# Optimization experiments

Measured on AMD Instinct MI355X. Metric: run time of the kernel, lower is better.

The kernel has to match this reference:

```python
import jax, jax.numpy as jnp
import numpy as np
import math

B, C, HH, WW = 4, 256, 64, 64
NUM_HEADS = 4
GROUPS = 8
EPS = 1e-5


def setup_inputs() -> dict:
    key = jax.random.key(0)
    k1, k2, k3 = jax.random.split(key, 3)
    x = jax.random.normal(k1, (B, C, HH, WW), dtype=jnp.float32)
    gn_w = jnp.ones((C,), dtype=jnp.float32)
    gn_b = jnp.zeros((C,), dtype=jnp.float32)
    qkv_w = jax.random.normal(k2, (3 * C, C), dtype=jnp.float32) * (1.0 / math.sqrt(C))
    qkv_b = jnp.zeros((3 * C,), dtype=jnp.float32)
    proj_w = jax.random.normal(k3, (C, C), dtype=jnp.float32) * (1.0 / math.sqrt(C))
    proj_b = jnp.zeros((C,), dtype=jnp.float32)
    return {"x": x, "gn_w": gn_w, "gn_b": gn_b, "qkv_w": qkv_w,
            "qkv_b": qkv_b, "proj_w": proj_w, "proj_b": proj_b}


def reference(x, gn_w, gn_b, qkv_w, qkv_b, proj_w, proj_b):
    b, c, h, w = x.shape
    nh = NUM_HEADS
    d = c // nh          # head dim = 64
    s = h * w            # sequence length = 4096

    # GroupNorm(8, c): normalize over (c//G, h, w) per group, biased variance
    xg = x.reshape(b, GROUPS, c // GROUPS, h, w)
    mu = xg.mean(axis=(2, 3, 4), keepdims=True)
    var = xg.var(axis=(2, 3, 4), keepdims=True)
    xn = ((xg - mu) * jax.lax.rsqrt(var + EPS)).reshape(b, c, h, w)
    xn = xn * gn_w[None, :, None, None] + gn_b[None, :, None, None]

    # 1x1 conv QKV == channel-wise matmul
    qkv = jnp.einsum('oc,bchw->bohw', qkv_w, xn) + qkv_b[None, :, None, None]
    qkv = qkv.reshape(b, 3, nh, d, s)
    q = jnp.transpose(qkv[:, 0], (0, 1, 3, 2))  # [b, nh, s, d]
    k = jnp.transpose(qkv[:, 1], (0, 1, 3, 2))
    v = jnp.transpose(qkv[:, 2], (0, 1, 3, 2))

    scale = 1.0 / math.sqrt(d)
    attn = jnp.einsum('bhqd,bhkd->bhqk', q, k) * scale  # [b, nh, s, s]
    attn = jax.nn.softmax(attn, axis=-1)
    out = jnp.einsum('bhqk,bhkd->bhqd', attn, v)        # [b, nh, s, d]

    out = jnp.transpose(out, (0, 1, 3, 2)).reshape(b, c, h, w)
    out = jnp.einsum('oc,bchw->bohw', proj_w, out) + proj_b[None, :, None, None]
    return out + x
```

## Files before the change

kernel.cpp:

```cpp
#include <hip/hip_runtime.h>
#include <hip/hip_bf16.h>

#define B_ 4
#define C_ 256
#define S_ 4096
#define NH_ 4
#define HD_ 64
#define LOG2E 1.4426950408889634f
#define QSC 0.18033688011112042f

typedef __attribute__((ext_vector_type(8))) short short8;
typedef __attribute__((ext_vector_type(4))) short short4v;
typedef __attribute__((ext_vector_type(4))) float f32x4;
typedef __attribute__((ext_vector_type(16))) float f32x16;
typedef __attribute__((ext_vector_type(4))) unsigned uint4v;

static __device__ __forceinline__ short f2bf(float f) {
  unsigned u = __builtin_bit_cast(unsigned, f);
  u += 0x7fffu + ((u >> 16) & 1u);
  return (short)(u >> 16);
}
static __device__ __forceinline__ float bf2f(short h) {
  unsigned u = ((unsigned)(unsigned short)h) << 16;
  return __builtin_bit_cast(float, u);
}

#if __has_builtin(__builtin_amdgcn_exp2f)
#define EXP2(x) __builtin_amdgcn_exp2f(x)
#else
#define EXP2(x) exp2f(x)
#endif

static __device__ __forceinline__ unsigned pkbf(float a, float b) {
  unsigned r;
  asm("v_cvt_pk_bf16_f32 %0, %1, %2" : "=v"(r) : "v"(a), "v"(b));
  return r;
}
static __device__ __forceinline__ void pl32swap(unsigned& a, unsigned& b) {
  asm volatile("v_permlane32_swap_b32 %0, %1" : "+v"(a), "+v"(b));
}
static __device__ __forceinline__ void gl_lds16(const short* g, char* l) {
  __builtin_amdgcn_global_load_lds(
      (const __attribute__((address_space(1))) void*)g,
      (__attribute__((address_space(3))) void*)l, 16, 0, 0);
}

__global__ __launch_bounds__(256) void k_pre(const float* __restrict__ x,
                                             const float* __restrict__ wq,
                                             const float* __restrict__ wp,
                                             float* __restrict__ part,
                                             short* __restrict__ oq,
                                             short* __restrict__ op) {
  int t = threadIdx.x;
  const float* p = x + (size_t)blockIdx.x * 16384;
  float s = 0.f, ss = 0.f;
  const float4* p4 = reinterpret_cast<const float4*>(p);
  for (int i = t; i < 4096; i += 256) {
    float4 v = p4[i];
    s += v.x + v.y + v.z + v.w;
    ss += v.x * v.x + v.y * v.y + v.z * v.z + v.w * v.w;
  }
  for (int m = 1; m < 64; m <<= 1) {
    s += __shfl_xor(s, m, 64);
    ss += __shfl_xor(ss, m, 64);
  }
  __shared__ float rs[4], rss[4];
  int w = t >> 6;
  if ((t & 63) == 0) { rs[w] = s; rss[w] = ss; }
  {
    int i = (blockIdx.x * 256 + t) * 4;
    const int n1 = 768 * 256;
    float sc = 1.f;
    const float* src;
    short* dst;
    if (i < n1) {
      src = wq + i; dst = oq + i;
      if (i < 256 * 256) sc = QSC;
    } else {
      src = wp + (i - n1); dst = op + (i - n1);
    }
    float4 v = *reinterpret_cast<const float4*>(src);
    short4v o;
    o[0] = f2bf(v.x * sc); o[1] = f2bf(v.y * sc);
    o[2] = f2bf(v.z * sc); o[3] = f2bf(v.w * sc);
    *reinterpret_cast<short4v*>(dst) = o;
  }
  __syncthreads();
  if (t == 0) {
    part[2 * blockIdx.x] = rs[0] + rs[1] + rs[2] + rs[3];
    part[2 * blockIdx.x + 1] = rss[0] + rss[1] + rss[2] + rss[3];
  }
}

__global__ __launch_bounds__(256) void k_gn_apply(const float* __restrict__ x,
                                                  const float* __restrict__ gw,
                                                  const float* __restrict__ gb,
                                                  const float* __restrict__ part,
                                                  short* __restrict__ xnt) {
  int st = blockIdx.x;
  int ct = blockIdx.y;
  int b = blockIdx.z;
  int t = threadIdx.x;
  __shared__ short T[64 * 72];
  __shared__ float smu[2], sri[2];
  int c0 = ct * 64, s0 = st * 64;
  if (t < 2) {
    int g = (c0 >> 5) + t;
    int base = b * 64 + g * 8;
    float s = 0.f, ss = 0.f;
    for (int j = 0; j < 8; j++) {
      s += part[2 * (base + j)];
      ss += part[2 * (base + j) + 1];
    }
    float inv = 1.f / (32.f * S_);
    float mu = s * inv;
    float var = ss * inv - mu * mu;
    smu[t] = mu;
    sri[t] = rsqrtf(var + 1e-5f);
  }
  __syncthreads();
  int r4 = t >> 4;
  int f4 = t & 15;
  for (int p = 0; p < 4; p++) {
    int r = p * 16 + r4;
    int c = c0 + r;
    int gl = r >> 5;
    float mu = smu[gl];
    float ri = sri[gl];
    float A = gw[c] * ri;
    float Bb = gb[c] - mu * A;
    float4 v = *reinterpret_cast<const float4*>(x + ((size_t)(b * C_ + c)) * S_ + s0 + f4 * 4);
    int sb = f4 * 4;
    T[(sb + 0) * 72 + r] = f2bf(v.x * A + Bb);
    T[(sb + 1) * 72 + r] = f2bf(v.y * A + Bb);
    T[(sb + 2) * 72 + r] = f2bf(v.z * A + Bb);
    T[(sb + 3) * 72 + r] = f2bf(v.w * A + Bb);
  }
  __syncthreads();
  for (int it = 0; it < 2; it++) {
    int cch = t + it * 256;
    int sl = cch >> 3, c8 = cch & 7;
    short8 v = *reinterpret_cast<short8*>(&T[sl * 72 + c8 * 8]);
    *reinterpret_cast<short8*>(xnt + ((size_t)(b * S_ + s0 + sl)) * C_ + c0 + c8 * 8) = v;
  }
}

template <int MODE, int NSP>
__global__ __launch_bounds__(256) void k_gemm(const short* __restrict__ Wbf,
                                              const short* __restrict__ Xt,
                                              const float* __restrict__ bias,
                                              const float* __restrict__ xres,
                                              short* __restrict__ q_sd,
                                              short* __restrict__ k_sd,
                                              short* __restrict__ v_ds,
                                              long op_stride,
                                              const float* __restrict__ lbufg,
                                              float* __restrict__ outp) {
  int tn = blockIdx.x;
  int tm = blockIdx.y;
  int b = blockIdx.z;
  int t = threadIdx.x;
  __shared__ short lds[4 * 64 * 72];
  char* glds = (char*)lds;
  short* Blp = lds + 4096;
  int w = t >> 6, lane = t & 63;
  int wr = w >> 1, wc = w & 1;
  int l15 = lane & 15, l4 = lane >> 4;
  int wbg = __builtin_amdgcn_readfirstlane(w) << 10;

  f32x4 acc[4][4];
  for (int m = 0; m < 4; m++)
    for (int n = 0; n < 4; n++)
      for (int j = 0; j < 4; j++) acc[m][n][j] = 0.f;

  const short* Arow = Wbf + (size_t)(tm * 128) * 256;
  const short* Brow = Xt + ((size_t)b * S_ + tn * 128) * 256;

  int r0 = t >> 2, c40 = t & 3;
  int sw0 = (c40 ^ ((r0 >> 1) & 3)) * 8;
  int r1 = (t + 256) >> 2;
  int sw1 = (c40 ^ ((r1 >> 1) & 3)) * 8;

  if (MODE == 0) {
    gl_lds16(Arow + (size_t)r0 * 256 + sw0, glds + wbg);
    gl_lds16(Arow + (size_t)r1 * 256 + sw1, glds + 4096 + wbg);
    gl_lds16(Brow + (size_t)r0 * 256 + sw0, glds + 8192 + wbg);
    gl_lds16(Brow + (size_t)r1 * 256 + sw1, glds + 12288 + wbg);
    asm volatile("s_waitcnt vmcnt(0)" ::: "memory");
    __builtin_amdgcn_s_barrier();
    asm volatile("" ::: "memory");
    for (int step = 0; step < 8; step++) {
      char* cb = glds + ((step & 1) << 14);
      if (step + 1 < 8) {
        char* nb = glds + (((step + 1) & 1) << 14);
        int kk = (step + 1) * 32;
        gl_lds16(Arow + (size_t)r0 * 256 + kk + sw0, nb + wbg);
        gl_lds16(Arow + (size_t)r1 * 256 + kk + sw1, nb + 4096 + wbg);
        gl_lds16(Brow + (size_t)r0 * 256 + kk + sw0, nb + 8192 + wbg);
        gl_lds16(Brow + (size_t)r1 * 256 + kk + sw1, nb + 12288 + wbg);
      }
      short8 af[4], bf[4];
      for (int mt = 0; mt < 4; mt++) {
        int row = wr * 64 + mt * 16 + l15;
        af[mt] = *reinterpret_cast<short8*>(cb + row * 64 + ((l4 ^ ((row >> 1) & 3)) << 4));
      }
      for (int nt = 0; nt < 4; nt++) {
        int row = wc * 64 + nt * 16 + l15;
        bf[nt] = *reinterpret_cast<short8*>(cb + 8192 + row * 64 + ((l4 ^ ((row >> 1) & 3)) << 4));
      }
      for (int mt = 0; mt < 4; mt++)
        for (int nt = 0; nt < 4; nt++)
          acc[mt][nt] =
              __builtin_amdgcn_mfma_f32_16x16x32_bf16(af[mt], bf[nt], acc[mt][nt], 0, 0, 0);
      if (step + 1 < 8) {
        asm volatile("s_waitcnt vmcnt(0)" ::: "memory");
        __builtin_amdgcn_s_barrier();
        asm volatile("" ::: "memory");
      }
    }
  } else {
    for (int kk = 0; kk < 256; kk += 32) {
      __syncthreads();
      gl_lds16(Arow + (size_t)r0 * 256 + kk + sw0, glds + wbg);
      gl_lds16(Arow + (size_t)r1 * 256 + kk + sw1, glds + 4096 + wbg);
      for (int i = 0; i < 2; i++) {
        int cch = t + i * 256;
        int r = cch >> 2, c4 = cch & 3;
        int c = kk + c4 * 8;
        int bh2 = b * 4 + (c >> 6);
        int d = c & 63;
        int s_glob = tn * 128 + r;
        size_t ro = ((size_t)bh2 * S_ + s_glob) * HD_ + d;
        float a8[8] = {0.f, 0.f, 0.f, 0.f, 0.f, 0.f, 0.f, 0.f};
        float l = 0.f;
#pragma unroll
        for (int i2 = 0; i2 < NSP; i2++) {
          short8 pv = *reinterpret_cast<const short8*>(Xt + (size_t)i2 * op_stride + ro);
#pragma unroll
          for (int j = 0; j < 8; j++) a8[j] += bf2f(pv[j]);
          l += lbufg[(size_t)(i2 * 16 + bh2) * S_ + s_glob];
        }
        float inv = 1.f / l;
        short8 vbv;
#pragma unroll
        for (int j = 0; j < 8; j++) vbv[j] = f2bf(a8[j] * inv);
        *reinterpret_cast<short8*>(&Blp[r * 40 + c4 * 8]) = vbv;
      }
      asm volatile("s_waitcnt vmcnt(0)" ::: "memory");
      __syncthreads();

      short8 af[4], bf[4];
      for (int mt = 0; mt < 4; mt++) {
        int row = wr * 64 + mt * 16 + l15;
        af[mt] = *reinterpret_cast<short8*>(glds + row * 64 + ((l4 ^ ((row >> 1) & 3)) << 4));
      }
      for (int nt = 0; nt < 4; nt++) {
        int row = wc * 64 + nt * 16 + l15;
        bf[nt] = *reinterpret_cast<short8*>(&Blp[row * 40 + l4 * 8]);
      }
      for (int mt = 0; mt < 4; mt++)
        for (int nt = 0; nt < 4; nt++)
          acc[mt][nt] =
              __builtin_amdgcn_mfma_f32_16x16x32_bf16(af[mt], bf[nt], acc[mt][nt], 0, 0, 0);
    }
  }
  __syncthreads();

  if (MODE == 0) {
    int o_base = tm * 128 + wr * 64;
    int tt = o_base >> 8;
    int h = (o_base >> 6) & 3;
    int s_base = tn * 128 + wc * 64;
    int bh = b * NH_ + h;
    if (tt == 2) {
      for (int mt = 0; mt < 4; mt++)
        for (int nt = 0; nt < 4; nt++)
          for (int i = 0; i < 4; i++) {
            int o = o_base + mt * 16 + l4 * 4 + i;
            int dd = o & 63;
            int s = s_base + nt * 16 + l15;
            float val = acc[mt][nt][i] + bias[o];
            v_ds[((size_t)bh * HD_ + dd) * S_ + s] = f2bf(val);
          }
    } else {
      float bsc = (tt == 0) ? QSC : 1.f;
      short* T = lds + w * (64 * 72);
      for (int mt = 0; mt < 4; mt++)
        for (int nt = 0; nt < 4; nt++)
          for (int i = 0; i < 4; i++) {
            int o = o_base + mt * 16 + l4 * 4 + i;
            int dd = mt * 16 + l4 * 4 + i;
            int sl = nt * 16 + l15;
            float val = acc[mt][nt][i] + bias[o] * bsc;
            T[sl * 72 + dd] = f2bf(val);
          }
      short* dst = (tt == 0) ? q_sd : k_sd;
      for (int it = 0; it < 8; it++) {
        int cch = lane + it * 64;
        int sl = cch >> 3, c8 = cch & 7;
        short8 v = *reinterpret_cast<short8*>(&T[sl * 72 + c8 * 8]);
        *reinterpret_cast<short8*>(dst + ((size_t)bh * S_ + s_base + sl) * HD_ + c8 * 8) = v;
      }
    }
  } else {
    for (int mt = 0; mt < 4; mt++) {
      int o = tm * 128 + wr * 64 + mt * 16 + l4 * 4;
      for (int nt = 0; nt < 4; nt++) {
        int s = tn * 128 + wc * 64 + nt * 16 + l15;
        for (int i = 0; i < 4; i++) {
          size_t off = ((size_t)(b * C_ + o + i)) * S_ + s;
          outp[off] = acc[mt][nt][i] + bias[o + i] + xres[off];
        }
      }
    }
  }
}

__global__ __launch_bounds__(256, 2) void k_attn(const short* __restrict__ q_sd,
                                                 const short* __restrict__ k_sd,
                                                 const short* __restrict__ v_ds,
                                                 short* __restrict__ op_base,
                                                 long op_stride,
                                                 float* __restrict__ lbuf,
                                                 int ntile) {
  int bid = blockIdx.x;
  int qt = bid >> 5;
  int bh = (bid >> 1) & 15;
  int sk = bid & 1;
  int t = threadIdx.x, w = t >> 6, lane = t & 63;
  int l31 = lane & 31, hi = lane >> 5, hi8 = hi * 8;
  int qb = qt * 256 + w * 64;

  __shared__ char smem[49152];

  int wb = __builtin_amdgcn_readfirstlane(w) << 10;

  int r8 = t >> 3, s8 = t & 7;
  int sw8 = (s8 ^ (r8 & 7)) * 8;
  const short* kb = k_sd + ((size_t)bh * S_ + (size_t)sk * ntile * 64) * HD_;
  const short* vbg = v_ds + (size_t)bh * HD_ * S_ + sk * ntile * 64;
  int koff0 = r8 * 64 + sw8;
  int koff1 = koff0 + 32 * 64;
  size_t voff0 = (size_t)r8 * S_ + sw8;
  size_t voff1 = voff0 + (size_t)32 * S_;

#define STAGE(bsel, ti)                                                        \
  do {                                                                         \
    const short* kt_ = kb + (size_t)(ti) * (64 * HD_);                         \
    const short* vt_ = vbg + (ti) * 64;                                        \
    char* lb_ = smem + ((bsel) << 14) + wb;                                    \
    gl_lds16(kt_ + koff0, lb_);                                                \
    gl_lds16(kt_ + koff1, lb_ + 4096);                                         \
    gl_lds16(vt_ + voff0, lb_ + 8192);                                         \
    gl_lds16(vt_ + voff1, lb_ + 12288);                                        \
  } while (0)

  const short* qpA = q_sd + ((size_t)bh * S_ + qb + l31) * HD_ + hi8;
  short8 qfA[4], qfB[4];
#pragma unroll
  for (int sl = 0; sl < 4; sl++) {
    qfA[sl] = *reinterpret_cast<const short8*>(qpA + sl * 16);
    qfB[sl] = *reinterpret_cast<const short8*>(qpA + 32 * HD_ + sl * 16);
  }

  int x7 = l31 & 7;
  int rb0 = l31 * 128;

  f32x16 OA0, OA1, OB0, OB1;
#pragma unroll
  for (int r = 0; r < 16; r++) { OA0[r] = 0.f; OA1[r] = 0.f; OB0[r] = 0.f; OB1[r] = 0.f; }
  float lA = 0.f, lB = 0.f;

  STAGE(0, 0);
  if (ntile > 1) STAGE(1, 1);
  asm volatile("s_waitcnt vmcnt(4)" ::: "memory");
  __builtin_amdgcn_s_barrier();
  asm volatile("" ::: "memory");

#define MKPA(pa, s0, s1)                                                       \
  do {                                                                         \
    unsigned c0 = pkbf(s0[0], s0[1]), c1 = pkbf(s0[2], s0[3]);                 \
    unsigned c2 = pkbf(s0[4], s0[5]), c3 = pkbf(s0[6], s0[7]);                 \
    pl32swap(c0, c2); pl32swap(c1, c3);                                        \
    uint4v u0; u0[0] = c0; u0[1] = c1; u0[2] = c2; u0[3] = c3;                 \
    pa[0] = __builtin_bit_cast(short8, u0);                                    \
    unsigned c4 = pkbf(s0[8], s0[9]), c5 = pkbf(s0[10], s0[11]);               \
    unsigned c6 = pkbf(s0[12], s0[13]), c7 = pkbf(s0[14], s0[15]);             \
    pl32swap(c4, c6); pl32swap(c5, c7);                                        \
    uint4v u1; u1[0] = c4; u1[1] = c5; u1[2] = c6; u1[3] = c7;                 \
    pa[1] = __builtin_bit_cast(short8, u1);                                    \
    unsigned d0 = pkbf(s1[0], s1[1]), d1 = pkbf(s1[2], s1[3]);                 \
    unsigned d2 = pkbf(s1[4], s1[5]), d3 = pkbf(s1[6], s1[7]);                 \
    pl32swap(d0, d2); pl32swap(d1, d3);                                        \
    uint4v u2; u2[0] = d0; u2[1] = d1; u2[2] = d2; u2[3] = d3;                 \
    pa[2] = __builtin_bit_cast(short8, u2);                                    \
    unsigned d4 = pkbf(s1[8], s1[9]), d5 = pkbf(s1[10], s1[11]);               \
    unsigned d6 = pkbf(s1[12], s1[13]), d7 = pkbf(s1[14], s1[15]);             \
    pl32swap(d4, d6); pl32swap(d5, d7);                                        \
    uint4v u3; u3[0] = d4; u3[1] = d5; u3[2] = d6; u3[3] = d7;                 \
    pa[3] = __builtin_bit_cast(short8, u3);                                    \
  } while (0)

  int cs = 0;
  for (int it = 0; it < ntile; it++) {
    char* cur = smem + (cs << 14);
    int ns = (cs == 2) ? 0 : cs + 1;
    int ps = (cs == 0) ? 2 : cs - 1;
    if (it + 2 < ntile) STAGE(ps, it + 2);

    f32x16 sA0, sA1, sB0, sB1;
#pragma unroll
    for (int r = 0; r < 16; r++) { sA0[r] = 0.f; sA1[r] = 0.f; sB0[r] = 0.f; sB1[r] = 0.f; }
    __builtin_amdgcn_s_setprio(1);
#pragma unroll
    for (int sl = 0; sl < 4; sl++) {
      int so = ((sl * 2 + hi) ^ x7) << 4;
      short8 kf0 = *reinterpret_cast<short8*>(cur + rb0 + so);
      short8 kf1 = *reinterpret_cast<short8*>(cur + 4096 + rb0 + so);
      sA0 = __builtin_amdgcn_mfma_f32_32x32x16_bf16(kf0, qfA[sl], sA0, 0, 0, 0);
      sB0 = __builtin_amdgcn_mfma_f32_32x32x16_bf16(kf0, qfB[sl], sB0, 0, 0, 0);
      sA1 = __builtin_amdgcn_mfma_f32_32x32x16_bf16(kf1, qfA[sl], sA1, 0, 0, 0);
      sB1 = __builtin_amdgcn_mfma_f32_32x32x16_bf16(kf1, qfB[sl], sB1, 0, 0, 0);
    }
    __builtin_amdgcn_s_setprio(0);

#pragma unroll
    for (int r = 0; r < 16; r++) sA0[r] = EXP2(sA0[r]);
#pragma unroll
    for (int r = 0; r < 16; r++) sA1[r] = EXP2(sA1[r]);
#pragma unroll
    for (int r = 0; r < 16; r++) sB0[r] = EXP2(sB0[r]);
#pragma unroll
    for (int r = 0; r < 16; r++) sB1[r] = EXP2(sB1[r]);
    {
      float a0 = 0.f, a1 = 0.f, a2 = 0.f, a3 = 0.f;
      float b0 = 0.f, b1 = 0.f, b2 = 0.f, b3 = 0.f;
#pragma unroll
      for (int r = 0; r < 16; r += 4) {
        a0 += sA0[r]; a1 += sA0[r + 1]; a2 += sA0[r + 2]; a3 += sA0[r + 3];
        a0 += sA1[r]; a1 += sA1[r + 1]; a2 += sA1[r + 2]; a3 += sA1[r + 3];
        b0 += sB0[r]; b1 += sB0[r + 1]; b2 += sB0[r + 2]; b3 += sB0[r + 3];
        b0 += sB1[r]; b1 += sB1[r + 1]; b2 += sB1[r + 2]; b3 += sB1[r + 3];
      }
      float rsA = (a0 + a1) + (a2 + a3);
      float rsB = (b0 + b1) + (b2 + b3);
      rsA += __shfl_xor(rsA, 32, 64);
      rsB += __shfl_xor(rsB, 32, 64);
      lA += rsA;
      lB += rsB;
    }

    short8 paA[4], paB[4];
    MKPA(paA, sA0, sA1);
    MKPA(paB, sB0, sB1);

    __builtin_amdgcn_s_setprio(1);
#pragma unroll
    for (int ks = 0; ks < 4; ks++) {
      int so = ((ks * 2 + hi) ^ x7) << 4;
      short8 vf0 = *reinterpret_cast<short8*>(cur + 8192 + rb0 + so);
      short8 vf1 = *reinterpret_cast<short8*>(cur + 12288 + rb0 + so);
      OA0 = __builtin_amdgcn_mfma_f32_32x32x16_bf16(vf0, paA[ks], OA0, 0, 0, 0);
      OB0 = __builtin_amdgcn_mfma_f32_32x32x16_bf16(vf0, paB[ks], OB0, 0, 0, 0);
      OA1 = __builtin_amdgcn_mfma_f32_32x32x16_bf16(vf1, paA[ks], OA1, 0, 0, 0);
      OB1 = __builtin_amdgcn_mfma_f32_32x32x16_bf16(vf1, paB[ks], OB1, 0, 0, 0);
    }
    __builtin_amdgcn_s_setprio(0);

    if (it + 1 < ntile) {
      if (it + 2 < ntile)
        asm volatile("s_waitcnt vmcnt(4)" ::: "memory");
      else
        asm volatile("s_waitcnt vmcnt(0)" ::: "memory");
      __builtin_amdgcn_s_barrier();
      asm volatile("" ::: "memory");
    }
    cs = ns;
  }

  short* optrA = op_base + (size_t)sk * op_stride + ((size_t)bh * S_ + qb + l31) * HD_;
  short* optrB = optrA + 32 * HD_;
#pragma unroll
  for (int qd = 0; qd < 4; qd++) {
    short4v a0, a1, b0v, b1v;
#pragma unroll
    for (int i = 0; i < 4; i++) {
      a0[i] = f2bf(OA0[qd * 4 + i]);
      a1[i] = f2bf(OA1[qd * 4 + i]);
      b0v[i] = f2bf(OB0[qd * 4 + i]);
      b1v[i] = f2bf(OB1[qd * 4 + i]);
    }
    int d0 = qd * 8 + hi * 4;
    *reinterpret_cast<short4v*>(optrA + d0) = a0;
    *reinterpret_cast<short4v*>(optrA + 32 + d0) = a1;
    *reinterpret_cast<short4v*>(optrB + d0) = b0v;
    *reinterpret_cast<short4v*>(optrB + 32 + d0) = b1v;
  }
  if (hi == 0) {
    lbuf[(size_t)(sk * 16 + bh) * S_ + qb + l31] = lA;
    lbuf[(size_t)(sk * 16 + bh) * S_ + qb + 32 + l31] = lB;
  }
#undef STAGE
#undef MKPA
}

extern "C" void kernel_launch(void* const* d_in, const int* in_sizes, int n_in,
                              void* d_out, int out_size, void* d_ws, size_t ws_size,
                              hipStream_t stream) {
  const float* x      = (const float*)d_in[0];
  const float* gn_w   = (const float*)d_in[1];
  const float* gn_b   = (const float*)d_in[2];
  const float* qkv_w  = (const float*)d_in[3];
  const float* qkv_b  = (const float*)d_in[4];
  const float* proj_w = (const float*)d_in[5];
  const float* proj_b = (const float*)d_in[6];
  char* ws = (char*)d_ws;
  float* part  = (float*)(ws + 2048);
  short* wqkv  = (short*)(ws + 4096);
  short* wproj = (short*)(ws + 397312);
  short* xnt   = (short*)(ws + 528384);
  short* q_sd  = (short*)(ws + 8916992);
  short* k_sd  = (short*)(ws + 17305600);
  short* v_ds  = (short*)(ws + 25694208);
  short* op_base = xnt;
  long op_stride = (42471424 - 528384) / 2;
  float* lbuf  = (float*)(ws + 50860032);
  float* outp  = (float*)d_out;

  k_pre<<<256, 256, 0, stream>>>(x, qkv_w, proj_w, part, wqkv, wproj);
  k_gn_apply<<<dim3(64, 4, 4), 256, 0, stream>>>(x, gn_w, gn_b, part, xnt);
  k_gemm<0, 0><<<dim3(32, 6, 4), 256, 0, stream>>>(wqkv, xnt, qkv_b, nullptr, q_sd, k_sd, v_ds,
                                                   0, nullptr, nullptr);
  k_attn<<<512, 256, 0, stream>>>(q_sd, k_sd, v_ds, op_base, op_stride, lbuf, 32);
  k_gemm<1, 2><<<dim3(32, 2, 4), 256, 0, stream>>>(wproj, op_base, proj_b, x, nullptr, nullptr,
                                                   nullptr, op_stride, lbuf, outp);
}
```

Baseline: 125.4 us.

## Interleave exp2 softmax with QK and PV MFMAs in attention inner loop

Splits the per-tile QK^T computation into two halves so the exp2 of the first half's scores is issued between the MFMAs of the second half. The second half's exp2 is likewise interleaved with the first half of the PV MFMAs. The aim is to hide transcendental VALU work behind matrix-core work instead of running them in sequence. It also moves the cross-half-wave row-sum shuffle out of the loop to a single reduction at the end. This changes instruction scheduling and register liveness, and may raise register pressure.

```diff
diff --git a/kernel.cpp b/kernel.cpp
--- a/kernel.cpp
+++ b/kernel.cpp
@@ -377,28 +377,18 @@
   __builtin_amdgcn_s_barrier();
   asm volatile("" ::: "memory");
 
-#define MKPA(pa, s0, s1)                                                       \
+#define MKPA2(pa0, pa1, s)                                                     \
   do {                                                                         \
-    unsigned c0 = pkbf(s0[0], s0[1]), c1 = pkbf(s0[2], s0[3]);                 \
-    unsigned c2 = pkbf(s0[4], s0[5]), c3 = pkbf(s0[6], s0[7]);                 \
+    unsigned c0 = pkbf(s[0], s[1]), c1 = pkbf(s[2], s[3]);                     \
+    unsigned c2 = pkbf(s[4], s[5]), c3 = pkbf(s[6], s[7]);                     \
     pl32swap(c0, c2); pl32swap(c1, c3);                                        \
     uint4v u0; u0[0] = c0; u0[1] = c1; u0[2] = c2; u0[3] = c3;                 \
-    pa[0] = __builtin_bit_cast(short8, u0);                                    \
-    unsigned c4 = pkbf(s0[8], s0[9]), c5 = pkbf(s0[10], s0[11]);               \
-    unsigned c6 = pkbf(s0[12], s0[13]), c7 = pkbf(s0[14], s0[15]);             \
+    pa0 = __builtin_bit_cast(short8, u0);                                      \
+    unsigned c4 = pkbf(s[8], s[9]), c5 = pkbf(s[10], s[11]);                   \
+    unsigned c6 = pkbf(s[12], s[13]), c7 = pkbf(s[14], s[15]);                 \
     pl32swap(c4, c6); pl32swap(c5, c7);                                        \
     uint4v u1; u1[0] = c4; u1[1] = c5; u1[2] = c6; u1[3] = c7;                 \
-    pa[1] = __builtin_bit_cast(short8, u1);                                    \
-    unsigned d0 = pkbf(s1[0], s1[1]), d1 = pkbf(s1[2], s1[3]);                 \
-    unsigned d2 = pkbf(s1[4], s1[5]), d3 = pkbf(s1[6], s1[7]);                 \
-    pl32swap(d0, d2); pl32swap(d1, d3);                                        \
-    uint4v u2; u2[0] = d0; u2[1] = d1; u2[2] = d2; u2[3] = d3;                 \
-    pa[2] = __builtin_bit_cast(short8, u2);                                    \
-    unsigned d4 = pkbf(s1[8], s1[9]), d5 = pkbf(s1[10], s1[11]);               \
-    unsigned d6 = pkbf(s1[12], s1[13]), d7 = pkbf(s1[14], s1[15]);             \
-    pl32swap(d4, d6); pl32swap(d5, d7);                                        \
-    uint4v u3; u3[0] = d4; u3[1] = d5; u3[2] = d6; u3[3] = d7;                 \
-    pa[3] = __builtin_bit_cast(short8, u3);                                    \
+    pa1 = __builtin_bit_cast(short8, u1);                                      \
   } while (0)
 
   int cs = 0;
@@ -408,62 +398,97 @@
     int ps = (cs == 0) ? 2 : cs - 1;
     if (it + 2 < ntile) STAGE(ps, it + 2);
 
-    f32x16 sA0, sA1, sB0, sB1;
-#pragma unroll
-    for (int r = 0; r < 16; r++) { sA0[r] = 0.f; sA1[r] = 0.f; sB0[r] = 0.f; sB1[r] = 0.f; }
+    f32x16 sA0, sB0;
+#pragma unroll
+    for (int r = 0; r < 16; r++) { sA0[r] = 0.f; sB0[r] = 0.f; }
     __builtin_amdgcn_s_setprio(1);
 #pragma unroll
     for (int sl = 0; sl < 4; sl++) {
       int so = ((sl * 2 + hi) ^ x7) << 4;
       short8 kf0 = *reinterpret_cast<short8*>(cur + rb0 + so);
-      short8 kf1 = *reinterpret_cast<short8*>(cur + 4096 + rb0 + so);
       sA0 = __builtin_amdgcn_mfma_f32_32x32x16_bf16(kf0, qfA[sl], sA0, 0, 0, 0);
       sB0 = __builtin_amdgcn_mfma_f32_32x32x16_bf16(kf0, qfB[sl], sB0, 0, 0, 0);
+    }
+
+    f32x16 sA1, sB1;
+#pragma unroll
+    for (int r = 0; r < 16; r++) { sA1[r] = 0.f; sB1[r] = 0.f; }
+#pragma unroll
+    for (int sl = 0; sl < 4; sl++) {
+      int so = ((sl * 2 + hi) ^ x7) << 4;
+      short8 kf1 = *reinterpret_cast<short8*>(cur + 4096 + rb0 + so);
       sA1 = __builtin_amdgcn_mfma_f32_32x32x16_bf16(kf1, qfA[sl], sA1, 0, 0, 0);
       sB1 = __builtin_amdgcn_mfma_f32_32x32x16_bf16(kf1, qfB[sl], sB1, 0, 0, 0);
+#pragma unroll
+      for (int j = 0; j < 4; j++) {
+        sA0[sl * 4 + j] = EXP2(sA0[sl * 4 + j]);
+        sB0[sl * 4 + j] = EXP2(sB0[sl * 4 + j]);
+      }
     }
     __builtin_amdgcn_s_setprio(0);
 
-#pragma unroll
-    for (int r = 0; r < 16; r++) sA0[r] = EXP2(sA0[r]);
-#pragma unroll
-    for (int r = 0; r < 16; r++) sA1[r] = EXP2(sA1[r]);
-#pragma unroll
-    for (int r = 0; r < 16; r++) sB0[r] = EXP2(sB0[r]);
-#pragma unroll
-    for (int r = 0; r < 16; r++) sB1[r] = EXP2(sB1[r]);
     {
       float a0 = 0.f, a1 = 0.f, a2 = 0.f, a3 = 0.f;
       float b0 = 0.f, b1 = 0.f, b2 = 0.f, b3 = 0.f;
 #pragma unroll
       for (int r = 0; r < 16; r += 4) {
         a0 += sA0[r]; a1 += sA0[r + 1]; a2 += sA0[r + 2]; a3 += sA0[r + 3];
-        a0 += sA1[r]; a1 += sA1[r + 1]; a2 += sA1[r + 2]; a3 += sA1[r + 3];
         b0 += sB0[r]; b1 += sB0[r + 1]; b2 += sB0[r + 2]; b3 += sB0[r + 3];
-        b0 += sB1[r]; b1 += sB1[r + 1]; b2 += sB1[r + 2]; b3 += sB1[r + 3];
-      }
-      float rsA = (a0 + a1) + (a2 + a3);
-      float rsB = (b0 + b1) + (b2 + b3);
-      rsA += __shfl_xor(rsA, 32, 64);
-      rsB += __shfl_xor(rsB, 32, 64);
-      lA += rsA;
-      lB += rsB;
-    }
-
-    short8 paA[4], paB[4];
-    MKPA(paA, sA0, sA1);
-    MKPA(paB, sB0, sB1);
+      }
+      lA += (a0 + a1) + (a2 + a3);
+      lB += (b0 + b1) + (b2 + b3);
+    }
+    short8 paA0, paA1, paB0, paB1;
+    MKPA2(paA0, paA1, sA0);
+    MKPA2(paB0, paB1, sB0);
 
     __builtin_amdgcn_s_setprio(1);
 #pragma unroll
-    for (int ks = 0; ks < 4; ks++) {
+    for (int ks = 0; ks < 2; ks++) {
       int so = ((ks * 2 + hi) ^ x7) << 4;
       short8 vf0 = *reinterpret_cast<short8*>(cur + 8192 + rb0 + so);
       short8 vf1 = *reinterpret_cast<short8*>(cur + 12288 + rb0 + so);
-      OA0 = __builtin_amdgcn_mfma_f32_32x32x16_bf16(vf0, paA[ks], OA0, 0, 0, 0);
-      OB0 = __builtin_amdgcn_mfma_f32_32x32x16_bf16(vf0, paB[ks], OB0, 0, 0, 0);
-      OA1 = __builtin_amdgcn_mfma_f32_32x32x16_bf16(vf1, paA[ks], OA1, 0, 0, 0);
-      OB1 = __builtin_amdgcn_mfma_f32_32x32x16_bf16(vf1, paB[ks], OB1, 0, 0, 0);
+      short8 pA = ks ? paA1 : paA0;
+      short8 pB = ks ? paB1 : paB0;
+      OA0 = __builtin_amdgcn_mfma_f32_32x32x16_bf16(vf0, pA, OA0, 0, 0, 0);
+      OB0 = __builtin_amdgcn_mfma_f32_32x32x16_bf16(vf0, pB, OB0, 0, 0, 0);
+      OA1 = __builtin_amdgcn_mfma_f32_32x32x16_bf16(vf1, pA, OA1, 0, 0, 0);
+      OB1 = __builtin_amdgcn_mfma_f32_32x32x16_bf16(vf1, pB, OB1, 0, 0, 0);
+#pragma unroll
+      for (int j = 0; j < 8; j++) {
+        sA1[ks * 8 + j] = EXP2(sA1[ks * 8 + j]);
+        sB1[ks * 8 + j] = EXP2(sB1[ks * 8 + j]);
+      }
+    }
+    __builtin_amdgcn_s_setprio(0);
+
+    {
+      float a0 = 0.f, a1 = 0.f, a2 = 0.f, a3 = 0.f;
+      float b0 = 0.f, b1 = 0.f, b2 = 0.f, b3 = 0.f;
+#pragma unroll
+      for (int r = 0; r < 16; r += 4) {
+        a0 += sA1[r]; a1 += sA1[r + 1]; a2 += sA1[r + 2]; a3 += sA1[r + 3];
+        b0 += sB1[r]; b1 += sB1[r + 1]; b2 += sB1[r + 2]; b3 += sB1[r + 3];
+      }
+      lA += (a0 + a1) + (a2 + a3);
+      lB += (b0 + b1) + (b2 + b3);
+    }
+    short8 paA2, paA3, paB2, paB3;
+    MKPA2(paA2, paA3, sA1);
+    MKPA2(paB2, paB3, sB1);
+
+    __builtin_amdgcn_s_setprio(1);
+#pragma unroll
+    for (int ks = 2; ks < 4; ks++) {
+      int so = ((ks * 2 + hi) ^ x7) << 4;
+      short8 vf0 = *reinterpret_cast<short8*>(cur + 8192 + rb0 + so);
+      short8 vf1 = *reinterpret_cast<short8*>(cur + 12288 + rb0 + so);
+      short8 pA = (ks == 2) ? paA2 : paA3;
+      short8 pB = (ks == 2) ? paB2 : paB3;
+      OA0 = __builtin_amdgcn_mfma_f32_32x32x16_bf16(vf0, pA, OA0, 0, 0, 0);
+      OB0 = __builtin_amdgcn_mfma_f32_32x32x16_bf16(vf0, pB, OB0, 0, 0, 0);
+      OA1 = __builtin_amdgcn_mfma_f32_32x32x16_bf16(vf1, pA, OA1, 0, 0, 0);
+      OB1 = __builtin_amdgcn_mfma_f32_32x32x16_bf16(vf1, pB, OB1, 0, 0, 0);
     }
     __builtin_amdgcn_s_setprio(0);
 
@@ -478,6 +503,8 @@
     cs = ns;
   }
 
+  lA += __shfl_xor(lA, 32, 64);
+  lB += __shfl_xor(lB, 32, 64);
   short* optrA = op_base + (size_t)sk * op_stride + ((size_t)bh * S_ + qb + l31) * HD_;
   short* optrB = optrA + 32 * HD_;
 #pragma unroll
@@ -501,7 +528,7 @@
     lbuf[(size_t)(sk * 16 + bh) * S_ + qb + 32 + l31] = lB;
   }
 #undef STAGE
-#undef MKPA
+#undef MKPA2
 }
 
 extern "C" void kernel_launch(void* const* d_in, const int* in_sizes, int n_in,
```

Measured after the change: 125.2 us. Within noise of the previous version (-0.1%).
